# Kernel optimization log

Measured on AMD Instinct MI355X. Metric: run time of the kernel, lower is better.

Reference implementation:

```python
import jax, jax.numpy as jnp
import numpy as np

NEG_SLOPE = 0.2


def setup_inputs() -> dict:
    key = jax.random.key(0)
    k1, k2, k3 = jax.random.split(key, 3)
    bs, n_agents, input_dim = 32, 512, 128
    n_heads, hidden_dim = 8, 64
    h = jax.random.normal(k1, (bs, n_agents, input_dim), dtype=jnp.float32)
    # Linear(input_dim, n_heads*hidden_dim, bias=False), stored as [in, out]
    W = jax.random.normal(k2, (input_dim, n_heads * hidden_dim), dtype=jnp.float32) * (1.0 / np.sqrt(input_dim))
    # xavier_uniform with gain=1.414 on shape (1, n_heads, 2*hidden_dim)
    fan = n_heads + 2 * hidden_dim
    bound = 1.414 * np.sqrt(6.0 / fan)
    att_a = jax.random.uniform(k3, (1, n_heads, 2 * hidden_dim), dtype=jnp.float32,
                               minval=-bound, maxval=bound)
    return {"h": h, "W": W, "att_a": att_a}


def reference(h, W, att_a):
    bs, n_agents, _ = h.shape
    n_heads = att_a.shape[1]
    hidden_dim = att_a.shape[2] // 2
    # h_prime: [bs, n_heads, n_agents, hidden_dim]
    h_prime = (h @ W).reshape(bs, n_agents, n_heads, hidden_dim).transpose(0, 2, 1, 3)
    # Additive score decomposes exactly: (a1.h_i + a2.h_j) == sum(cat(h_i,h_j)*a)
    a_src = att_a[0, :, :hidden_dim]   # [n_heads, hidden_dim]
    a_dst = att_a[0, :, hidden_dim:]   # [n_heads, hidden_dim]
    e_src = jnp.einsum('bhnd,hd->bhn', h_prime, a_src)  # score contribution of node i (row)
    e_dst = jnp.einsum('bhnd,hd->bhn', h_prime, a_dst)  # contribution of node j (col)
    e = e_src[:, :, :, None] + e_dst[:, :, None, :]     # [bs, n_heads, n, n]
    e = jnp.where(e >= 0, e, NEG_SLOPE * e)             # leaky_relu(0.2)
    attention = jax.nn.softmax(e, axis=-1)
    h_new = jnp.einsum('bhnm,bhmd->bhnd', attention, h_prime)
    return jax.nn.elu(h_new)
```

## Files before the change

kernel.cpp:

```cpp
#include <hip/hip_runtime.h>

#define BS 32
#define NA 512
#define ID 128
#define NH 8
#define HD 64
#define NHD 512
#define NEG 0.2f
#define NC 32
#define CH 16
#define NW 8
#define BPAD 136

typedef short bf16x8 __attribute__((ext_vector_type(8)));
typedef float f32x4 __attribute__((ext_vector_type(4)));

__device__ inline unsigned f2bf_bits(float x) {
  unsigned u = __float_as_uint(x);
  return (u + 0x7FFFu + ((u >> 16) & 1u)) >> 16;
}

__device__ inline void split8(const float4& x, const float4& y,
                              bf16x8& hi, bf16x8& lo) {
  float f[8] = {x.x, x.y, x.z, x.w, y.x, y.y, y.z, y.w};
  #pragma unroll
  for (int j = 0; j < 8; ++j) {
    unsigned hb = f2bf_bits(f[j]);
    float r = f[j] - __uint_as_float(hb << 16);
    unsigned lb = f2bf_bits(r);
    hi[j] = (short)hb;
    lo[j] = (short)lb;
  }
}

__global__ __launch_bounds__(256, 4) void k1_mfma(
    const float* __restrict__ h, const float* __restrict__ W,
    float* __restrict__ hp) {
  __shared__ unsigned short Bhi[64 * BPAD];
  __shared__ unsigned short Blo[64 * BPAD];

  int blk = blockIdx.x;
  int mt = blk >> 3;
  int n0 = (blk & 7) * 64;
  int m0 = mt * 128;
  int b = mt >> 2;
  int nbase = (mt & 3) * 128;
  int head = n0 >> 6;
  int t = threadIdx.x;
  int lane = t & 63, w = t >> 6;
  int q = lane >> 4, ml = lane & 15;

  {
    int c = t & 63, kq = t >> 6;
    const float* wsrc = W + (size_t)kq * 32 * NHD + n0 + c;
    #pragma unroll 4
    for (int kk = 0; kk < 32; ++kk) {
      int k = kq * 32 + kk;
      float x = wsrc[(size_t)kk * NHD];
      unsigned hb = f2bf_bits(x);
      float r = x - __uint_as_float(hb << 16);
      Bhi[c * BPAD + k] = (unsigned short)hb;
      Blo[c * BPAD + k] = (unsigned short)f2bf_bits(r);
    }
  }
  __syncthreads();

  f32x4 acc[2][4];
  #pragma unroll
  for (int mf = 0; mf < 2; ++mf)
    #pragma unroll
    for (int nf = 0; nf < 4; ++nf)
      acc[mf][nf] = (f32x4){0.f, 0.f, 0.f, 0.f};

  const float* A0 = h + (size_t)(m0 + w * 32 + ml) * ID;

  #pragma unroll
  for (int ks = 0; ks < 4; ++ks) {
    int ko = ks * 32 + q * 8;
    bf16x8 ah[2], al[2];
    #pragma unroll
    for (int mf = 0; mf < 2; ++mf) {
      const float* ap = A0 + mf * 16 * ID + ko;
      float4 f0 = *(const float4*)ap;
      float4 f1 = *(const float4*)(ap + 4);
      split8(f0, f1, ah[mf], al[mf]);
    }
    #pragma unroll
    for (int nf = 0; nf < 4; ++nf) {
      int bo = (nf * 16 + ml) * BPAD + ko;
      bf16x8 bh = *(const bf16x8*)&Bhi[bo];
      bf16x8 bl = *(const bf16x8*)&Blo[bo];
      #pragma unroll
      for (int mf = 0; mf < 2; ++mf) {
        acc[mf][nf] = __builtin_amdgcn_mfma_f32_16x16x32_bf16(ah[mf], bh, acc[mf][nf], 0, 0, 0);
        acc[mf][nf] = __builtin_amdgcn_mfma_f32_16x16x32_bf16(ah[mf], bl, acc[mf][nf], 0, 0, 0);
        acc[mf][nf] = __builtin_amdgcn_mfma_f32_16x16x32_bf16(al[mf], bh, acc[mf][nf], 0, 0, 0);
      }
    }
  }

  {
    float* ob = hp + (((size_t)b * NH + head) * NA + nbase + w * 32) * HD + ml;
    #pragma unroll
    for (int mf = 0; mf < 2; ++mf)
      #pragma unroll
      for (int nf = 0; nf < 4; ++nf)
        #pragma unroll
        for (int r = 0; r < 4; ++r)
          ob[(size_t)(mf * 16 + q * 4 + r) * HD + nf * 16] = acc[mf][nf][r];
  }
}

__global__ __launch_bounds__(512, 2) void k2_fused(
    const float* __restrict__ hp, const float* __restrict__ att,
    float* __restrict__ out) {
  __shared__ float tv[NA]; __shared__ int tpm[NA];
  __shared__ float sv[NA]; __shared__ int spm[NA];
  __shared__ float wp[NA]; __shared__ float wn[NA];
  __shared__ float rawP8[NW * 64]; __shared__ float rawN8[NW * 64];
  __shared__ float sufPc[(NW + 1) * 64]; __shared__ float preNc[(NW + 1) * 64];
  __shared__ float zps[NA + 1]; __shared__ float znp[NA + 1];
  __shared__ float szP[NC]; __shared__ float szN[NC];
  __shared__ float sufZ[NC + 1]; __shared__ float preZ[NC + 1];
  __shared__ float4 abi[NA];
  __shared__ int jsr[NA];
  __shared__ int Earr[NA];
  __shared__ float asrc[HD]; __shared__ float adst[HD];

  int bh = blockIdx.x;
  int head = bh & (NH - 1);
  int t = threadIdx.x;
  int lane = t & 63, w = t >> 6;
  const float* vbase = hp + (size_t)bh * NA * HD;

  if (t < 2 * HD) {
    float a = att[head * 2 * HD + t];
    if (t < HD) asrc[t] = a; else adst[t - HD] = a;
  }
  __syncthreads();

  float vt, vs; int it = t, is_ = t;
  {
    const float4* vr = (const float4*)(vbase + (size_t)t * HD);
    float s0 = 0.f, s1 = 0.f, t0 = 0.f, t1 = 0.f;
    #pragma unroll
    for (int j = 0; j < HD / 4; j += 2) {
      float4 v0 = vr[j], v1 = vr[j + 1];
      s0 += v0.x*asrc[4*j+0] + v0.y*asrc[4*j+1] + v0.z*asrc[4*j+2] + v0.w*asrc[4*j+3];
      t0 += v0.x*adst[4*j+0] + v0.y*adst[4*j+1] + v0.z*adst[4*j+2] + v0.w*adst[4*j+3];
      s1 += v1.x*asrc[4*j+4] + v1.y*asrc[4*j+5] + v1.z*asrc[4*j+6] + v1.w*asrc[4*j+7];
      t1 += v1.x*adst[4*j+4] + v1.y*adst[4*j+5] + v1.z*adst[4*j+6] + v1.w*adst[4*j+7];
    }
    vs = s0 + s1; vt = t0 + t1;
  }

  for (int size = 2; size <= NA; size <<= 1) {
    bool dirAsc = ((t & size) == 0);
    for (int stride = size >> 1; stride > 0; stride >>= 1) {
      float pt, ps; int pit, pis;
      if (stride >= 64) {
        tv[t] = vt; tpm[t] = it; sv[t] = vs; spm[t] = is_;
        __syncthreads();
        pt = tv[t ^ stride]; pit = tpm[t ^ stride];
        ps = sv[t ^ stride]; pis = spm[t ^ stride];
        __syncthreads();
      } else {
        pt = __shfl_xor(vt, stride, 64); pit = __shfl_xor(it, stride, 64);
        ps = __shfl_xor(vs, stride, 64); pis = __shfl_xor(is_, stride, 64);
      }
      bool mn = (((t & stride) == 0) == dirAsc);
      if (mn ? (pt < vt) : (pt > vt)) { vt = pt; it = pit; }
      if (mn ? (ps < vs) : (ps > vs)) { vs = ps; is_ = pis; }
    }
  }
  tv[t] = vt; tpm[t] = it; sv[t] = vs; spm[t] = is_;
  __syncthreads();

  float cmax = fmaxf(tv[NA - 1], 0.f);
  float amax = fmaxf(sv[NA - 1], 0.f);
  wp[t] = __expf(vt - cmax);
  wn[t] = __expf(NEG * vt - cmax);
  __syncthreads();

  {
    float aP = 0.f, aN = 0.f;
    #pragma unroll
    for (int jj = 0; jj < 64; ++jj) {
      int j = (w << 6) + jj;
      float vv = vbase[(size_t)tpm[j] * HD + lane];
      aP += wp[j] * vv;
      aN += wn[j] * vv;
    }
    rawP8[(w << 6) + lane] = aP;
    rawN8[(w << 6) + lane] = aN;
  }
  __syncthreads();

  if (t < 64) {
    int d = t; float run = 0.f;
    sufPc[NW * 64 + d] = 0.f;
    for (int ww = NW - 1; ww >= 0; --ww) {
      run += rawP8[ww * 64 + d]; sufPc[ww * 64 + d] = run;
    }
  } else if (t < 128) {
    int d = t - 64; float run = 0.f;
    for (int ww = 0; ww <= NW; ++ww) {
      preNc[ww * 64 + d] = run;
      if (ww < NW) run += rawN8[ww * 64 + d];
    }
  } else if (t < 160) {
    int c = t - 128; float a = 0.f;
    for (int j = c * CH; j < c * CH + CH; ++j) a += wp[j];
    szP[c] = a;
  } else if (t < 192) {
    int c = t - 160; float a = 0.f;
    for (int j = c * CH; j < c * CH + CH; ++j) a += wn[j];
    szN[c] = a;
  }
  __syncthreads();

  if (t == 0) {
    float run = 0.f; sufZ[NC] = 0.f;
    for (int cc = NC - 1; cc >= 0; --cc) { run += szP[cc]; sufZ[cc] = run; }
  } else if (t == 1) {
    float run = 0.f;
    for (int cc = 0; cc <= NC; ++cc) { preZ[cc] = run; if (cc < NC) run += szN[cc]; }
  }
  __syncthreads();

  {
    int ch = t >> 4;
    float a = 0.f;
    for (int k = t; k < ch * CH + CH; ++k) a += wp[k];
    zps[t] = a + sufZ[ch + 1];
    float b2 = 0.f;
    for (int k = ch * CH; k < t; ++k) b2 += wn[k];
    znp[t] = preZ[ch] + b2;
    if (t == 0) { zps[NA] = 0.f; znp[NA] = preZ[NC]; }
  }
  __syncthreads();

  {
    float A = __expf(vs - amax);
    float B = __expf(NEG * vs - amax);
    float key = -vs;
    int lo = 0, hi = NA;
    while (lo < hi) { int mid = (lo + hi) >> 1; if (tv[mid] < key) lo = mid + 1; else hi = mid; }
    float den = A * zps[lo] + B * znp[lo];
    float4 qv; qv.x = A; qv.y = B; qv.z = 1.f / den; qv.w = __int_as_float(is_);
    abi[t] = qv;
    jsr[t] = lo;
  }
  __syncthreads();

  {
    int lo = 0, hi = NA;
    while (lo < hi) { int mid = (lo + hi) >> 1; if (jsr[mid] > t) lo = mid + 1; else hi = mid; }
    Earr[t] = lo;
  }
  __syncthreads();

  {
    float sufPv = sufPc[w * 64 + lane];
    float preSeedN = preNc[w * 64 + lane];
    float runN = 0.f;
    size_t obase = (size_t)bh * NA * HD + lane;
    int jb = w << 6;
    int eprev = (w == 0) ? NA : Earr[jb - 1];
    float vv0 = vbase[(size_t)tpm[jb] * HD + lane];
    float vv1 = vbase[(size_t)tpm[jb + 1] * HD + lane];
    #pragma unroll 1
    for (int jj = 0; jj < 64; ++jj) {
      int j = jb + jj;
      float vv = vv0;
      vv0 = vv1;
      if (jj < 62) vv1 = vbase[(size_t)tpm[j + 2] * HD + lane];
      int ecur = Earr[j];
      float preNv = preSeedN + runN;
      for (int r = ecur; r < eprev; ++r) {
        float4 qv = abi[r];
        float x = (qv.x * sufPv + qv.y * preNv) * qv.z;
        int orow = __float_as_int(qv.w);
        out[obase + (size_t)orow * HD] = x > 0.f ? x : __expf(x) - 1.f;
      }
      sufPv -= wp[j] * vv;
      runN  += wn[j] * vv;
      eprev = ecur;
    }
    if (w == NW - 1) {
      float preNv = preSeedN + runN;
      for (int r = 0; r < eprev; ++r) {
        float4 qv = abi[r];
        float x = (qv.y * preNv) * qv.z;
        int orow = __float_as_int(qv.w);
        out[obase + (size_t)orow * HD] = x > 0.f ? x : __expf(x) - 1.f;
      }
    }
  }
}

extern "C" void kernel_launch(void* const* d_in, const int* in_sizes, int n_in,
                              void* d_out, int out_size, void* d_ws, size_t ws_size,
                              hipStream_t stream) {
  const float* h   = (const float*)d_in[0];
  const float* W   = (const float*)d_in[1];
  const float* att = (const float*)d_in[2];
  float* out = (float*)d_out;
  float* hp  = (float*)d_ws;

  k1_mfma <<<dim3(1024),    dim3(256), 0, stream>>>(h, W, hp);
  k2_fused<<<dim3(BS * NH), dim3(512), 0, stream>>>(hp, att, out);
}
```

Before: 140.2 us.

## Split fused attention kernel into sort, chunk-sum and apply kernels

Computes the per-node source and destination scores inside the GEMM epilogue with warp shuffles, so the second stage no longer re-reads h_prime to form dot products. The former single 512-thread block per (batch, head) is split into a sort kernel, a 64-thread chunk partial-sum kernel and a 64-thread apply kernel, with 2048 blocks for the last two. The aim is more parallelism and better load balance in the scan and apply phases. In exchange it adds two kernel launches and global-memory round trips for the sorted indices, weights, prefix data and partial sums.

```diff
diff --git a/kernel.cpp b/kernel.cpp
--- a/kernel.cpp
+++ b/kernel.cpp
@@ -9,7 +9,7 @@
 #define NEG 0.2f
 #define NC 32
 #define CH 16
-#define NW 8
+#define NCH 8
 #define BPAD 136
 
 typedef short bf16x8 __attribute__((ext_vector_type(8)));
@@ -35,7 +35,8 @@
 
 __global__ __launch_bounds__(256, 4) void k1_mfma(
     const float* __restrict__ h, const float* __restrict__ W,
-    float* __restrict__ hp) {
+    const float* __restrict__ att, float* __restrict__ hp,
+    float* __restrict__ sG, float* __restrict__ tG) {
   __shared__ unsigned short Bhi[64 * BPAD];
   __shared__ unsigned short Blo[64 * BPAD];
 
@@ -109,50 +110,56 @@
         for (int r = 0; r < 4; ++r)
           ob[(size_t)(mf * 16 + q * 4 + r) * HD + nf * 16] = acc[mf][nf][r];
   }
-}
-
-__global__ __launch_bounds__(512, 2) void k2_fused(
-    const float* __restrict__ hp, const float* __restrict__ att,
-    float* __restrict__ out) {
+
+  {
+    float a_s[4], a_d[4];
+    #pragma unroll
+    for (int nf = 0; nf < 4; ++nf) {
+      a_s[nf] = att[head * 128 + nf * 16 + ml];
+      a_d[nf] = att[head * 128 + 64 + nf * 16 + ml];
+    }
+    #pragma unroll
+    for (int mf = 0; mf < 2; ++mf) {
+      #pragma unroll
+      for (int r = 0; r < 4; ++r) {
+        float sp = 0.f, tp = 0.f;
+        #pragma unroll
+        for (int nf = 0; nf < 4; ++nf) {
+          float c = acc[mf][nf][r];
+          sp += c * a_s[nf]; tp += c * a_d[nf];
+        }
+        #pragma unroll
+        for (int m = 1; m < 16; m <<= 1) {
+          sp += __shfl_xor(sp, m, 64);
+          tp += __shfl_xor(tp, m, 64);
+        }
+        if (ml == 0) {
+          int row = nbase + w * 32 + mf * 16 + q * 4 + r;
+          size_t o = ((size_t)b * NH + head) * NA + row;
+          sG[o] = sp; tG[o] = tp;
+        }
+      }
+    }
+  }
+}
+
+__global__ __launch_bounds__(512, 2) void k2a_sort(
+    const float* __restrict__ sG, const float* __restrict__ tG,
+    int* __restrict__ tpmG, float* __restrict__ wpG, float* __restrict__ wnG,
+    float4* __restrict__ abiG, int* __restrict__ EarrG) {
   __shared__ float tv[NA]; __shared__ int tpm[NA];
   __shared__ float sv[NA]; __shared__ int spm[NA];
   __shared__ float wp[NA]; __shared__ float wn[NA];
-  __shared__ float rawP8[NW * 64]; __shared__ float rawN8[NW * 64];
-  __shared__ float sufPc[(NW + 1) * 64]; __shared__ float preNc[(NW + 1) * 64];
   __shared__ float zps[NA + 1]; __shared__ float znp[NA + 1];
   __shared__ float szP[NC]; __shared__ float szN[NC];
   __shared__ float sufZ[NC + 1]; __shared__ float preZ[NC + 1];
-  __shared__ float4 abi[NA];
   __shared__ int jsr[NA];
-  __shared__ int Earr[NA];
-  __shared__ float asrc[HD]; __shared__ float adst[HD];
 
   int bh = blockIdx.x;
-  int head = bh & (NH - 1);
   int t = threadIdx.x;
-  int lane = t & 63, w = t >> 6;
-  const float* vbase = hp + (size_t)bh * NA * HD;
-
-  if (t < 2 * HD) {
-    float a = att[head * 2 * HD + t];
-    if (t < HD) asrc[t] = a; else adst[t - HD] = a;
-  }
-  __syncthreads();
-
-  float vt, vs; int it = t, is_ = t;
-  {
-    const float4* vr = (const float4*)(vbase + (size_t)t * HD);
-    float s0 = 0.f, s1 = 0.f, t0 = 0.f, t1 = 0.f;
-    #pragma unroll
-    for (int j = 0; j < HD / 4; j += 2) {
-      float4 v0 = vr[j], v1 = vr[j + 1];
-      s0 += v0.x*asrc[4*j+0] + v0.y*asrc[4*j+1] + v0.z*asrc[4*j+2] + v0.w*asrc[4*j+3];
-      t0 += v0.x*adst[4*j+0] + v0.y*adst[4*j+1] + v0.z*adst[4*j+2] + v0.w*adst[4*j+3];
-      s1 += v1.x*asrc[4*j+4] + v1.y*asrc[4*j+5] + v1.z*asrc[4*j+6] + v1.w*asrc[4*j+7];
-      t1 += v1.x*adst[4*j+4] + v1.y*adst[4*j+5] + v1.z*adst[4*j+6] + v1.w*adst[4*j+7];
-    }
-    vs = s0 + s1; vt = t0 + t1;
-  }
+
+  float vt = tG[(size_t)bh * NA + t]; int it = t;
+  float vs = sG[(size_t)bh * NA + t]; int is_ = t;
 
   for (int size = 2; size <= NA; size <<= 1) {
     bool dirAsc = ((t & size) == 0);
@@ -178,42 +185,20 @@
 
   float cmax = fmaxf(tv[NA - 1], 0.f);
   float amax = fmaxf(sv[NA - 1], 0.f);
-  wp[t] = __expf(vt - cmax);
-  wn[t] = __expf(NEG * vt - cmax);
-  __syncthreads();
-
-  {
-    float aP = 0.f, aN = 0.f;
-    #pragma unroll
-    for (int jj = 0; jj < 64; ++jj) {
-      int j = (w << 6) + jj;
-      float vv = vbase[(size_t)tpm[j] * HD + lane];
-      aP += wp[j] * vv;
-      aN += wn[j] * vv;
-    }
-    rawP8[(w << 6) + lane] = aP;
-    rawN8[(w << 6) + lane] = aN;
-  }
-  __syncthreads();
-
-  if (t < 64) {
-    int d = t; float run = 0.f;
-    sufPc[NW * 64 + d] = 0.f;
-    for (int ww = NW - 1; ww >= 0; --ww) {
-      run += rawP8[ww * 64 + d]; sufPc[ww * 64 + d] = run;
-    }
-  } else if (t < 128) {
-    int d = t - 64; float run = 0.f;
-    for (int ww = 0; ww <= NW; ++ww) {
-      preNc[ww * 64 + d] = run;
-      if (ww < NW) run += rawN8[ww * 64 + d];
-    }
-  } else if (t < 160) {
-    int c = t - 128; float a = 0.f;
+  float wpt = __expf(vt - cmax);
+  float wnt = __expf(NEG * vt - cmax);
+  wp[t] = wpt; wn[t] = wnt;
+  tpmG[(size_t)bh * NA + t] = it;
+  wpG[(size_t)bh * NA + t] = wpt;
+  wnG[(size_t)bh * NA + t] = wnt;
+  __syncthreads();
+
+  if (t < NC) {
+    int c = t; float a = 0.f;
     for (int j = c * CH; j < c * CH + CH; ++j) a += wp[j];
     szP[c] = a;
-  } else if (t < 192) {
-    int c = t - 160; float a = 0.f;
+  } else if (t < 2 * NC) {
+    int c = t - NC; float a = 0.f;
     for (int j = c * CH; j < c * CH + CH; ++j) a += wn[j];
     szN[c] = a;
   }
@@ -228,6 +213,7 @@
   }
   __syncthreads();
 
+  int myjs;
   {
     int ch = t >> 4;
     float a = 0.f;
@@ -237,64 +223,99 @@
     for (int k = ch * CH; k < t; ++k) b2 += wn[k];
     znp[t] = preZ[ch] + b2;
     if (t == 0) { zps[NA] = 0.f; znp[NA] = preZ[NC]; }
-  }
-  __syncthreads();
-
-  {
-    float A = __expf(vs - amax);
-    float B = __expf(NEG * vs - amax);
     float key = -vs;
     int lo = 0, hi = NA;
     while (lo < hi) { int mid = (lo + hi) >> 1; if (tv[mid] < key) lo = mid + 1; else hi = mid; }
-    float den = A * zps[lo] + B * znp[lo];
+    jsr[t] = lo; myjs = lo;
+  }
+  __syncthreads();
+
+  {
+    float A = __expf(vs - amax);
+    float B = __expf(NEG * vs - amax);
+    float den = A * zps[myjs] + B * znp[myjs];
     float4 qv; qv.x = A; qv.y = B; qv.z = 1.f / den; qv.w = __int_as_float(is_);
-    abi[t] = qv;
-    jsr[t] = lo;
-  }
-  __syncthreads();
-
-  {
+    abiG[(size_t)bh * NA + t] = qv;
     int lo = 0, hi = NA;
     while (lo < hi) { int mid = (lo + hi) >> 1; if (jsr[mid] > t) lo = mid + 1; else hi = mid; }
-    Earr[t] = lo;
-  }
-  __syncthreads();
-
-  {
-    float sufPv = sufPc[w * 64 + lane];
-    float preSeedN = preNc[w * 64 + lane];
-    float runN = 0.f;
-    size_t obase = (size_t)bh * NA * HD + lane;
-    int jb = w << 6;
-    int eprev = (w == 0) ? NA : Earr[jb - 1];
-    float vv0 = vbase[(size_t)tpm[jb] * HD + lane];
-    float vv1 = vbase[(size_t)tpm[jb + 1] * HD + lane];
-    #pragma unroll 1
-    for (int jj = 0; jj < 64; ++jj) {
-      int j = jb + jj;
-      float vv = vv0;
-      vv0 = vv1;
-      if (jj < 62) vv1 = vbase[(size_t)tpm[j + 2] * HD + lane];
-      int ecur = Earr[j];
-      float preNv = preSeedN + runN;
-      for (int r = ecur; r < eprev; ++r) {
-        float4 qv = abi[r];
-        float x = (qv.x * sufPv + qv.y * preNv) * qv.z;
-        int orow = __float_as_int(qv.w);
-        out[obase + (size_t)orow * HD] = x > 0.f ? x : __expf(x) - 1.f;
-      }
-      sufPv -= wp[j] * vv;
-      runN  += wn[j] * vv;
-      eprev = ecur;
-    }
-    if (w == NW - 1) {
-      float preNv = preSeedN + runN;
-      for (int r = 0; r < eprev; ++r) {
-        float4 qv = abi[r];
-        float x = (qv.y * preNv) * qv.z;
-        int orow = __float_as_int(qv.w);
-        out[obase + (size_t)orow * HD] = x > 0.f ? x : __expf(x) - 1.f;
-      }
+    EarrG[(size_t)bh * NA + t] = lo;
+  }
+}
+
+__global__ __launch_bounds__(64) void k2b_sums(
+    const float* __restrict__ hp, const int* __restrict__ tpmG,
+    const float* __restrict__ wpG, const float* __restrict__ wnG,
+    float* __restrict__ rawPG, float* __restrict__ rawNG) {
+  __shared__ float wpS[64], wnS[64]; __shared__ int tpS[64];
+  int blk = blockIdx.x;
+  int bh = blk >> 3, c = blk & 7;
+  int lane = threadIdx.x;
+  size_t base = (size_t)bh * NA + c * 64;
+  wpS[lane] = wpG[base + lane];
+  wnS[lane] = wnG[base + lane];
+  tpS[lane] = tpmG[base + lane];
+  __syncthreads();
+  const float* vb = hp + (size_t)bh * NA * HD;
+  float aP = 0.f, aN = 0.f;
+  #pragma unroll 4
+  for (int jj = 0; jj < 64; ++jj) {
+    float vv = vb[(size_t)tpS[jj] * HD + lane];
+    aP += wpS[jj] * vv;
+    aN += wnS[jj] * vv;
+  }
+  rawPG[base + lane] = aP;
+  rawNG[base + lane] = aN;
+}
+
+__global__ __launch_bounds__(64) void k2d_apply(
+    const float* __restrict__ hp, const int* __restrict__ tpmG,
+    const float* __restrict__ wpG, const float* __restrict__ wnG,
+    const int* __restrict__ EarrG, const float4* __restrict__ abiG,
+    const float* __restrict__ rawPG, const float* __restrict__ rawNG,
+    float* __restrict__ out) {
+  __shared__ float wpS[64], wnS[64]; __shared__ int tpS[64]; __shared__ int eS[64];
+  int blk = blockIdx.x;
+  int bh = blk >> 3, c = blk & 7;
+  int lane = threadIdx.x;
+  size_t base = (size_t)bh * NA + c * 64;
+  wpS[lane] = wpG[base + lane];
+  wnS[lane] = wnG[base + lane];
+  tpS[lane] = tpmG[base + lane];
+  eS[lane]  = EarrG[base + lane];
+  int eprev = (c == 0) ? NA : EarrG[base - 1];
+  size_t rb = (size_t)bh * NA + lane;
+  float sufPv = 0.f;
+  for (int cc = NCH - 1; cc >= c; --cc) sufPv += rawPG[rb + cc * 64];
+  float preSeedN = 0.f;
+  for (int cc = 0; cc < c; ++cc) preSeedN += rawNG[rb + cc * 64];
+  __syncthreads();
+
+  const float* vb = hp + (size_t)bh * NA * HD;
+  const float4* ab = abiG + (size_t)bh * NA;
+  float runN = 0.f;
+  size_t obase = (size_t)bh * NA * HD + lane;
+  #pragma unroll 2
+  for (int jj = 0; jj < 64; ++jj) {
+    float vv = vb[(size_t)tpS[jj] * HD + lane];
+    int ecur = eS[jj];
+    float preNv = preSeedN + runN;
+    for (int r = ecur; r < eprev; ++r) {
+      float4 qv = ab[r];
+      float x = (qv.x * sufPv + qv.y * preNv) * qv.z;
+      int orow = __float_as_int(qv.w);
+      out[obase + (size_t)orow * HD] = x > 0.f ? x : __expf(x) - 1.f;
+    }
+    sufPv -= wpS[jj] * vv;
+    runN  += wnS[jj] * vv;
+    eprev = ecur;
+  }
+  if (c == NCH - 1) {
+    float preNv = preSeedN + runN;
+    for (int r = 0; r < eprev; ++r) {
+      float4 qv = ab[r];
+      float x = (qv.y * preNv) * qv.z;
+      int orow = __float_as_int(qv.w);
+      out[obase + (size_t)orow * HD] = x > 0.f ? x : __expf(x) - 1.f;
     }
   }
 }
@@ -306,8 +327,22 @@
   const float* W   = (const float*)d_in[1];
   const float* att = (const float*)d_in[2];
   float* out = (float*)d_out;
-  float* hp  = (float*)d_ws;
-
-  k1_mfma <<<dim3(1024),    dim3(256), 0, stream>>>(h, W, hp);
-  k2_fused<<<dim3(BS * NH), dim3(512), 0, stream>>>(hp, att, out);
-}
+
+  const size_t R = (size_t)BS * NH * NA;
+  float* hp    = (float*)d_ws;
+  float* sG    = hp + (size_t)BS * NH * NA * HD;
+  float* tG    = sG + R;
+  float* wpG   = tG + R;
+  float* wnG   = wpG + R;
+  int*   tpmG  = (int*)(wnG + R);
+  float4* abiG = (float4*)(tpmG + R);
+  int*   EarrG = (int*)(abiG + R);
+  float* rawPG = (float*)(EarrG + R);
+  float* rawNG = rawPG + R;
+
+  k1_mfma <<<dim3(1024),       dim3(256), 0, stream>>>(h, W, att, hp, sG, tG);
+  k2a_sort<<<dim3(BS * NH),    dim3(512), 0, stream>>>(sG, tG, tpmG, wpG, wnG, abiG, EarrG);
+  k2b_sums<<<dim3(BS * NH * 8), dim3(64), 0, stream>>>(hp, tpmG, wpG, wnG, rawPG, rawNG);
+  k2d_apply<<<dim3(BS * NH * 8), dim3(64), 0, stream>>>(hp, tpmG, wpG, wnG, EarrG, abiG,
+                                                        rawPG, rawNG, out);
+}
```

New measurement: 152.9 us. 9.0% more time.
